# Kernel optimization log

Hardware: AMD Instinct MI355X
Metric: run time of the kernel (lower is better)

The kernel has to match this reference:

```python
import jax, jax.numpy as jnp
import numpy as np

B, N, E, DIN, H1, H2, DOUT = 2, 20000, 320000, 128, 256, 256, 128


def setup_inputs() -> dict:
    key = jax.random.key(0)
    ks = jax.random.split(key, 9)
    X = jax.random.normal(ks[0], (B, N, DIN), dtype=jnp.float32)
    edge_index = jax.random.randint(ks[1], (2, E), 0, N, dtype=jnp.int32)
    def lin(k, fan_in, fan_out):
        lim = 1.0 / np.sqrt(fan_in)
        return jax.random.uniform(k, (fan_in, fan_out), jnp.float32, -lim, lim)
    W1 = lin(ks[2], DIN, H1); b1 = jnp.zeros((H1,), jnp.float32)
    W2 = lin(ks[3], H1, H2);  b2 = jnp.zeros((H2,), jnp.float32)
    W3 = lin(ks[4], H2, DOUT); b3 = jnp.zeros((DOUT,), jnp.float32)
    prelu_a = jnp.array(0.25, jnp.float32)  # PReLU default single shared param
    return dict(X=X, W1=W1, b1=b1, W2=W2, b2=b2, W3=W3, b3=b3,
                prelu_a=prelu_a, edge_index=edge_index)


def reference(X, W1, b1, W2, b2, W3, b3, prelu_a, edge_index):
    src, dst = edge_index[0], edge_index[1]
    n = X.shape[1]
    # GCN symmetric normalization with self-loops: deg = in-degree + 1
    deg = jax.ops.segment_sum(jnp.ones_like(src, X.dtype), dst, num_segments=n) + 1.0
    dinv = jax.lax.rsqrt(deg)                      # [N]
    norm_e = dinv[src] * dinv[dst]                 # [E] edge norm
    norm_self = dinv * dinv                        # [N] self-loop norm

    def gcn(x, W, b):
        h = x @ W                                  # [N, F_out]
        agg = jax.ops.segment_sum(h[src] * norm_e[:, None], dst, num_segments=n)
        agg = agg + h * norm_self[:, None]         # add self-loop message
        return agg + b

    def prelu(x):
        return jnp.where(x >= 0, x, prelu_a * x)

    def single(x):  # x: [N, DIN]
        x = prelu(gcn(x, W1, b1))
        x = prelu(gcn(x, W2, b2))
        return gcn(x, W3, b3)

    return jax.vmap(single)(X)                     # [B, N, DOUT]
```

## Files before the change

### kernel.cpp

```cpp
#include <hip/hip_runtime.h>

#define NB 20000
#define EB 320000
#define DIN 128
#define H1D 256
#define H2D 256
#define DOUTD 128
#define SCAN_BLOCKS ((NB + 255) / 256)
#define NPB 80


__global__ void zero_kernel(int* __restrict__ p, int n) {
    int t = blockIdx.x * blockDim.x + threadIdx.x;
    if (t < n) p[t] = 0;
}

__global__ void hist_kernel(const int* __restrict__ dst, int* __restrict__ bins) {
    int t = blockIdx.x * blockDim.x + threadIdx.x;
    if (t < EB) atomicAdd(&bins[dst[t]], 1);
}

__global__ __launch_bounds__(256) void scanA_kernel(const int* __restrict__ bins,
                                                    int* __restrict__ loc,
                                                    int* __restrict__ blksum) {
    __shared__ int s[256];
    int t = threadIdx.x;
    int i = blockIdx.x * 256 + t;
    int v = (i < NB) ? bins[i] : 0;
    s[t] = v;
    __syncthreads();
    for (int off = 1; off < 256; off <<= 1) {
        int u = (t >= off) ? s[t - off] : 0;
        __syncthreads();
        s[t] += u;
        __syncthreads();
    }
    if (i < NB) loc[i] = s[t] - v;
    if (t == 255) blksum[blockIdx.x] = s[255];
}

__global__ __launch_bounds__(128) void scanB_kernel(int* __restrict__ blksum) {
    __shared__ int s[128];
    int t = threadIdx.x;
    int v = (t < SCAN_BLOCKS) ? blksum[t] : 0;
    s[t] = v;
    __syncthreads();
    for (int off = 1; off < 128; off <<= 1) {
        int u = (t >= off) ? s[t - off] : 0;
        __syncthreads();
        s[t] += u;
        __syncthreads();
    }
    if (t < SCAN_BLOCKS) blksum[t] = s[t] - v;
}

__global__ __launch_bounds__(256) void scanC_kernel(const int* __restrict__ bins,
                                                    const int* __restrict__ loc,
                                                    const int* __restrict__ blksum,
                                                    int* __restrict__ rs,
                                                    int* __restrict__ cursor,
                                                    float* __restrict__ dinv) {
    int i = blockIdx.x * 256 + threadIdx.x;
    if (i < NB) {
        int r = loc[i] + blksum[blockIdx.x];
        rs[i] = r;
        cursor[i] = r;
        dinv[i] = rsqrtf((float)bins[i] + 1.0f);
    }
    if (i == 0) rs[NB] = EB;
}

__global__ void scatter_kernel(const int* __restrict__ src, const int* __restrict__ dst,
                               const float* __restrict__ dinv,
                               int* __restrict__ cursor, int2* __restrict__ edges) {
    int t = blockIdx.x * blockDim.x + threadIdx.x;
    if (t < EB) {
        int d = dst[t], s = src[t];
        int p = atomicAdd(&cursor[d], 1);
        edges[p] = make_int2(s, __float_as_int(dinv[s] * dinv[d]));
    }
}


template <int F, bool SPLIT_IN, bool SPLIT_OUT, bool BIAS, bool PRELU>
__global__ __launch_bounds__(256) void aggs_kernel(
    const float* __restrict__ h, float* __restrict__ out,
    const int* __restrict__ rs, const int2* __restrict__ edges,
    const float* __restrict__ dinv, const float* __restrict__ bias,
    const float* __restrict__ pa) {
    constexpr int SLW = F / 8;
    constexpr int ROWF = 2 * SLW;
    constexpr int EPW = 64 / ROWF;
    constexpr int GSTRIDE = SPLIT_IN ? F : 2 * F;
    constexpr int OSTRIDE = SPLIT_OUT ? F : 2 * F;

    const int s = blockIdx.x & 7;
    const int chunk = blockIdx.x >> 3;
    const int wid = threadIdx.x >> 6;
    const int lane = threadIdx.x & 63;
    const int half = lane / ROWF;
    const int li = lane % ROWF;
    const int b = li / SLW;
    const int c = li % SLW;
    const int foff = s * SLW + c;

    const float* gbase = h + (SPLIT_IN ? (size_t)b * NB * F : (size_t)b * F) + foff;
    float* obase = out + (SPLIT_OUT ? (size_t)b * NB * F : (size_t)b * F) + foff;
    const float pav = PRELU ? *pa : 0.0f;
    const float bval = BIAS ? bias[foff] : 0.0f;

    const int npw = NPB / 4;
    int n = chunk * NPB + wid * npw;
    for (int j = 0; j < npw; ++j, ++n) {
        int e0 = __builtin_amdgcn_readfirstlane(rs[n]);
        int e1 = __builtin_amdgcn_readfirstlane(rs[n + 1]);
        float acc0 = 0.0f, acc1 = 0.0f;
        int e = e0;
        for (; e + 2 * EPW <= e1; e += 2 * EPW) {
            int2 ed0 = edges[e + half];
            int2 ed1 = edges[e + EPW + half];
            float t0 = gbase[(size_t)ed0.x * GSTRIDE];
            float t1 = gbase[(size_t)ed1.x * GSTRIDE];
            acc0 = fmaf(t0, __int_as_float(ed0.y), acc0);
            acc1 = fmaf(t1, __int_as_float(ed1.y), acc1);
        }
        for (; e < e1; e += EPW) {
            int my_e = e + half;
            bool valid = (my_e < e1);
            int2 ed = edges[valid ? my_e : (e1 - 1)];
            float t = gbase[(size_t)ed.x * GSTRIDE];
            float w = valid ? __int_as_float(ed.y) : 0.0f;
            acc0 = fmaf(t, w, acc0);
        }
        float acc = acc0 + acc1;
        if (EPW == 2) acc += __shfl_xor(acc, 32, 64);
        float dv = dinv[n];
        float ts = gbase[(size_t)n * GSTRIDE];
        float r = fmaf(ts, dv * dv, acc);
        if (BIAS) r += bval;
        if (PRELU) r = (r >= 0.0f) ? r : pav * r;
        if (EPW == 1 || half == 0) obase[(size_t)n * OSTRIDE] = r;
    }
}

template <bool BIAS, bool PRELU>
__global__ __launch_bounds__(256) void gemm_kernel(const float* __restrict__ A, int M, int K,
                                                   const float* __restrict__ W, int Nc,
                                                   const float* __restrict__ bias,
                                                   const float* __restrict__ pa,
                                                   float* __restrict__ C) {
    __shared__ alignas(16) float As[16][132];
    __shared__ alignas(16) float Bs[16][68];
    int t = threadIdx.x;
    int bm = blockIdx.x * 128;
    int bn = blockIdx.y * 64;
    int tx = t & 15, ty = t >> 4;
    int m0 = ty * 8, n0 = tx * 4;
    int ar = t >> 2, ac4 = (t & 3) * 4;
    int br = t >> 4, bc4 = (t & 15) * 4;

    float acc[8][4] = {};

    for (int k0 = 0; k0 < K; k0 += 16) {
        float4 a0 = make_float4(0.f, 0.f, 0.f, 0.f), a1 = a0;
        int r0 = bm + ar, r1 = bm + ar + 64;
        if (r0 < M) a0 = *(const float4*)&A[(size_t)r0 * K + k0 + ac4];
        if (r1 < M) a1 = *(const float4*)&A[(size_t)r1 * K + k0 + ac4];
        As[ac4 + 0][ar] = a0.x; As[ac4 + 1][ar] = a0.y;
        As[ac4 + 2][ar] = a0.z; As[ac4 + 3][ar] = a0.w;
        As[ac4 + 0][ar + 64] = a1.x; As[ac4 + 1][ar + 64] = a1.y;
        As[ac4 + 2][ar + 64] = a1.z; As[ac4 + 3][ar + 64] = a1.w;
        float4 bv = *(const float4*)&W[(size_t)(k0 + br) * Nc + bn + bc4];
        *(float4*)&Bs[br][bc4] = bv;
        __syncthreads();
#pragma unroll
        for (int k = 0; k < 16; ++k) {
            float4 av0 = *(const float4*)&As[k][m0];
            float4 av1 = *(const float4*)&As[k][m0 + 4];
            float4 bv4 = *(const float4*)&Bs[k][n0];
            float a_[8] = {av0.x, av0.y, av0.z, av0.w, av1.x, av1.y, av1.z, av1.w};
            float b_[4] = {bv4.x, bv4.y, bv4.z, bv4.w};
#pragma unroll
            for (int i = 0; i < 8; ++i)
#pragma unroll
                for (int j = 0; j < 4; ++j)
                    acc[i][j] = fmaf(a_[i], b_[j], acc[i][j]);
        }
        __syncthreads();
    }

    float pav = 0.0f;
    if (PRELU) pav = *pa;
#pragma unroll
    for (int i = 0; i < 8; ++i) {
        int row = bm + m0 + i;
        if (row < M) {
            float v[4];
#pragma unroll
            for (int j = 0; j < 4; ++j) {
                float x = acc[i][j];
                if (BIAS) x += bias[bn + n0 + j];
                if (PRELU) x = (x >= 0.0f) ? x : pav * x;
                v[j] = x;
            }
            *(float4*)&C[(size_t)row * Nc + bn + n0] = make_float4(v[0], v[1], v[2], v[3]);
        }
    }
}


static inline char* carve(char*& p, size_t bytes) {
    char* r = p;
    p += (bytes + 255) & ~(size_t)255;
    return r;
}

extern "C" void kernel_launch(void* const* d_in, const int* in_sizes, int n_in,
                              void* d_out, int out_size, void* d_ws, size_t ws_size,
                              hipStream_t stream) {
    const float* X  = (const float*)d_in[0];
    const float* W1 = (const float*)d_in[1];
    const float* b1 = (const float*)d_in[2];
    const float* W2 = (const float*)d_in[3];
    const float* b2 = (const float*)d_in[4];
    const float* W3 = (const float*)d_in[5];
    const float* b3 = (const float*)d_in[6];
    const float* pa = (const float*)d_in[7];
    const int* ei   = (const int*)d_in[8];
    const int* src = ei;
    const int* dst = ei + EB;
    float* out = (float*)d_out;

    char* p = (char*)d_ws;
    int* bins    = (int*)carve(p, NB * sizeof(int));
    int* loc     = (int*)carve(p, NB * sizeof(int));
    int* blksum  = (int*)carve(p, 128 * sizeof(int));
    int* rs      = (int*)carve(p, (NB + 1) * sizeof(int));
    int* cursor  = (int*)carve(p, NB * sizeof(int));
    int2* edges  = (int2*)carve(p, EB * sizeof(int2));
    float* dinv  = (float*)carve(p, NB * sizeof(float));
    float* bufA  = (float*)carve(p, (size_t)2 * NB * 256 * sizeof(float));
    float* bufB  = (float*)carve(p, (size_t)2 * NB * 256 * sizeof(float));

    const int M = 2 * NB;

    zero_kernel<<<SCAN_BLOCKS, 256, 0, stream>>>(bins, NB);
    hist_kernel<<<(EB + 255) / 256, 256, 0, stream>>>(dst, bins);
    scanA_kernel<<<SCAN_BLOCKS, 256, 0, stream>>>(bins, loc, blksum);
    scanB_kernel<<<1, 128, 0, stream>>>(blksum);
    scanC_kernel<<<SCAN_BLOCKS, 256, 0, stream>>>(bins, loc, blksum, rs, cursor, dinv);
    scatter_kernel<<<(EB + 255) / 256, 256, 0, stream>>>(src, dst, dinv, cursor, edges);

    const int aggGrid = (NB / NPB) * 8;

    aggs_kernel<128, true, false, false, false><<<aggGrid, 256, 0, stream>>>(
        X, bufA, rs, edges, dinv, nullptr, nullptr);
    gemm_kernel<true, true><<<dim3((M + 127) / 128, H1D / 64), 256, 0, stream>>>(
        bufA, M, DIN, W1, H1D, b1, pa, bufB);

    gemm_kernel<false, false><<<dim3((M + 127) / 128, H2D / 64), 256, 0, stream>>>(
        bufB, M, H1D, W2, H2D, nullptr, nullptr, bufA);
    aggs_kernel<256, false, false, true, true><<<aggGrid, 256, 0, stream>>>(
        bufA, bufB, rs, edges, dinv, b2, pa);

    gemm_kernel<false, false><<<dim3((M + 127) / 128, DOUTD / 64), 256, 0, stream>>>(
        bufB, M, H2D, W3, DOUTD, nullptr, nullptr, bufA);
    aggs_kernel<128, false, true, true, false><<<aggGrid, 256, 0, stream>>>(
        bufA, out, rs, edges, dinv, b3, nullptr);
}
```

Measured before the change: 492.1 us.

## Restructure aggregation: 32-wide feature slices per batch, 4-way edge unroll, phased launches

Replaces the sliced aggregation kernel with one where each block handles a single batch and a 32-float feature slice, and each wave splits edges across two half-waves with four independent accumulators. Blocks now cover 20 nodes instead of 80, and the 256-feature layer is split into two launches (phase 0/1) so each launch touches half the feature columns. The goal is contiguous 128-byte gathers per edge, more memory-level parallelism, and a smaller per-launch working set for better cache reuse. In exchange it adds an extra kernel launch and reads the edge list more times.

```diff
diff --git a/kernel.cpp b/kernel.cpp
--- a/kernel.cpp
+++ b/kernel.cpp
@@ -7,7 +7,6 @@
 #define H2D 256
 #define DOUTD 128
 #define SCAN_BLOCKS ((NB + 255) / 256)
-#define NPB 80
 
 
 __global__ void zero_kernel(int* __restrict__ p, int n) {
@@ -83,63 +82,69 @@
 
 
 template <int F, bool SPLIT_IN, bool SPLIT_OUT, bool BIAS, bool PRELU>
-__global__ __launch_bounds__(256) void aggs_kernel(
+__global__ __launch_bounds__(256) void aggv_kernel(
     const float* __restrict__ h, float* __restrict__ out,
     const int* __restrict__ rs, const int2* __restrict__ edges,
     const float* __restrict__ dinv, const float* __restrict__ bias,
-    const float* __restrict__ pa) {
-    constexpr int SLW = F / 8;
-    constexpr int ROWF = 2 * SLW;
-    constexpr int EPW = 64 / ROWF;
-    constexpr int GSTRIDE = SPLIT_IN ? F : 2 * F;
-    constexpr int OSTRIDE = SPLIT_OUT ? F : 2 * F;
-
-    const int s = blockIdx.x & 7;
+    const float* __restrict__ pa, int phase) {
+    const int ss = blockIdx.x & 7;
     const int chunk = blockIdx.x >> 3;
     const int wid = threadIdx.x >> 6;
     const int lane = threadIdx.x & 63;
-    const int half = lane / ROWF;
-    const int li = lane % ROWF;
-    const int b = li / SLW;
-    const int c = li % SLW;
-    const int foff = s * SLW + c;
-
-    const float* gbase = h + (SPLIT_IN ? (size_t)b * NB * F : (size_t)b * F) + foff;
-    float* obase = out + (SPLIT_OUT ? (size_t)b * NB * F : (size_t)b * F) + foff;
+    const int li = lane & 31;
+    const int eh = lane >> 5;
+    const int b = ss >> 2;
+    const int c32 = (ss & 3) + phase * 4;
+    const int fo = c32 * 32 + li;
+
+    constexpr size_t GS = SPLIT_IN ? F : 2 * F;
+    constexpr size_t OS = SPLIT_OUT ? F : 2 * F;
+    const float* gb = h + (SPLIT_IN ? (size_t)b * NB * F : (size_t)b * F) + fo;
+    float* ob = out + (SPLIT_OUT ? (size_t)b * NB * F : (size_t)b * F) + fo;
+
     const float pav = PRELU ? *pa : 0.0f;
-    const float bval = BIAS ? bias[foff] : 0.0f;
-
-    const int npw = NPB / 4;
-    int n = chunk * NPB + wid * npw;
-    for (int j = 0; j < npw; ++j, ++n) {
-        int e0 = __builtin_amdgcn_readfirstlane(rs[n]);
-        int e1 = __builtin_amdgcn_readfirstlane(rs[n + 1]);
-        float acc0 = 0.0f, acc1 = 0.0f;
+    const float bval = BIAS ? bias[fo] : 0.0f;
+
+    int n = chunk * 20 + wid * 5;
+    int e1n = __builtin_amdgcn_readfirstlane(rs[n]);
+    for (int j = 0; j < 5; ++j, ++n) {
+        int e0 = e1n;
+        e1n = __builtin_amdgcn_readfirstlane(rs[n + 1]);
+        int e1 = e1n;
+        float a0 = 0.f, a1 = 0.f, a2 = 0.f, a3 = 0.f;
         int e = e0;
-        for (; e + 2 * EPW <= e1; e += 2 * EPW) {
-            int2 ed0 = edges[e + half];
-            int2 ed1 = edges[e + EPW + half];
-            float t0 = gbase[(size_t)ed0.x * GSTRIDE];
-            float t1 = gbase[(size_t)ed1.x * GSTRIDE];
-            acc0 = fmaf(t0, __int_as_float(ed0.y), acc0);
-            acc1 = fmaf(t1, __int_as_float(ed1.y), acc1);
-        }
-        for (; e < e1; e += EPW) {
-            int my_e = e + half;
-            bool valid = (my_e < e1);
-            int2 ed = edges[valid ? my_e : (e1 - 1)];
-            float t = gbase[(size_t)ed.x * GSTRIDE];
-            float w = valid ? __int_as_float(ed.y) : 0.0f;
-            acc0 = fmaf(t, w, acc0);
-        }
-        float acc = acc0 + acc1;
-        if (EPW == 2) acc += __shfl_xor(acc, 32, 64);
+        for (; e + 8 <= e1; e += 8) {
+            int2 r0 = edges[e + eh];
+            int2 r1 = edges[e + 2 + eh];
+            int2 r2 = edges[e + 4 + eh];
+            int2 r3 = edges[e + 6 + eh];
+            float t0 = gb[(size_t)r0.x * GS];
+            float t1 = gb[(size_t)r1.x * GS];
+            float t2 = gb[(size_t)r2.x * GS];
+            float t3 = gb[(size_t)r3.x * GS];
+            a0 = fmaf(t0, __int_as_float(r0.y), a0);
+            a1 = fmaf(t1, __int_as_float(r1.y), a1);
+            a2 = fmaf(t2, __int_as_float(r2.y), a2);
+            a3 = fmaf(t3, __int_as_float(r3.y), a3);
+        }
+        for (; e + 2 <= e1; e += 2) {
+            int2 r0 = edges[e + eh];
+            a0 = fmaf(gb[(size_t)r0.x * GS], __int_as_float(r0.y), a0);
+        }
+        if (e < e1) {
+            int my = e + eh;
+            bool valid = (my < e1);
+            int2 r0 = edges[valid ? my : e];
+            float w = valid ? __int_as_float(r0.y) : 0.0f;
+            a0 = fmaf(gb[(size_t)r0.x * GS], w, a0);
+        }
+        float acc = (a0 + a1) + (a2 + a3);
+        acc += __shfl_xor(acc, 32, 64);
         float dv = dinv[n];
-        float ts = gbase[(size_t)n * GSTRIDE];
-        float r = fmaf(ts, dv * dv, acc);
+        float r = fmaf(gb[(size_t)n * GS], dv * dv, acc);
         if (BIAS) r += bval;
         if (PRELU) r = (r >= 0.0f) ? r : pav * r;
-        if (EPW == 1 || half == 0) obase[(size_t)n * OSTRIDE] = r;
+        if (eh == 0) ob[(size_t)n * OS] = r;
     }
 }
 
@@ -243,6 +248,7 @@
     float* bufB  = (float*)carve(p, (size_t)2 * NB * 256 * sizeof(float));
 
     const int M = 2 * NB;
+    const int AGGV = 1000 * 8;
 
     zero_kernel<<<SCAN_BLOCKS, 256, 0, stream>>>(bins, NB);
     hist_kernel<<<(EB + 255) / 256, 256, 0, stream>>>(dst, bins);
@@ -251,20 +257,23 @@
     scanC_kernel<<<SCAN_BLOCKS, 256, 0, stream>>>(bins, loc, blksum, rs, cursor, dinv);
     scatter_kernel<<<(EB + 255) / 256, 256, 0, stream>>>(src, dst, dinv, cursor, edges);
 
-    const int aggGrid = (NB / NPB) * 8;
-
-    aggs_kernel<128, true, false, false, false><<<aggGrid, 256, 0, stream>>>(
-        X, bufA, rs, edges, dinv, nullptr, nullptr);
+    aggv_kernel<128, true, false, false, false><<<AGGV, 256, 0, stream>>>(
+        X, bufA, rs, edges, dinv, nullptr, nullptr, 0);
+
     gemm_kernel<true, true><<<dim3((M + 127) / 128, H1D / 64), 256, 0, stream>>>(
         bufA, M, DIN, W1, H1D, b1, pa, bufB);
 
     gemm_kernel<false, false><<<dim3((M + 127) / 128, H2D / 64), 256, 0, stream>>>(
         bufB, M, H1D, W2, H2D, nullptr, nullptr, bufA);
-    aggs_kernel<256, false, false, true, true><<<aggGrid, 256, 0, stream>>>(
-        bufA, bufB, rs, edges, dinv, b2, pa);
+
+    aggv_kernel<256, false, false, true, true><<<AGGV, 256, 0, stream>>>(
+        bufA, bufB, rs, edges, dinv, b2, pa, 0);
+    aggv_kernel<256, false, false, true, true><<<AGGV, 256, 0, stream>>>(
+        bufA, bufB, rs, edges, dinv, b2, pa, 1);
 
     gemm_kernel<false, false><<<dim3((M + 127) / 128, DOUTD / 64), 256, 0, stream>>>(
         bufB, M, H2D, W3, DOUTD, nullptr, nullptr, bufA);
-    aggs_kernel<128, false, true, true, false><<<aggGrid, 256, 0, stream>>>(
-        bufA, out, rs, edges, dinv, b3, nullptr);
-}
+
+    aggv_kernel<128, false, true, true, false><<<AGGV, 256, 0, stream>>>(
+        bufA, out, rs, edges, dinv, b3, nullptr, 0);
+}
```

New measurement: 490.7 us. About the same (-0.3%).
